# Kernel tuning notes

Hardware: AMD Instinct MI355X
Metric: run time of the kernel (lower is better)

Reference implementation:

```python
import jax, jax.numpy as jnp
import numpy as np

# Block structure (mirrors init_kwargs)
K = 8            # number of blocks
BLK = 1024       # per-block in/out width
TOTAL = K * BLK  # total_dim = 8192
INPUT_IDX = [(i * BLK, (i + 1) * BLK) for i in range(K)]
OUTPUT_IDX = [(((i + 1) % K) * BLK, ((i + 1) % K + 1) * BLK) for i in range(K)]
BATCH = 4096


def setup_inputs() -> dict:
    key = jax.random.key(0)
    k1, k2, k3, k4 = jax.random.split(key, 4)
    x = jax.random.normal(k1, (BATCH, TOTAL), dtype=jnp.float32)
    v = jax.random.normal(k2, (BATCH, TOTAL), dtype=jnp.float32)
    # Per-block Linear params; nn.Linear default init ~ U(-1/sqrt(in), 1/sqrt(in))
    bound = 1.0 / np.sqrt(BLK)
    W = jax.random.uniform(k3, (K, BLK, BLK), dtype=jnp.float32, minval=-bound, maxval=bound)  # [K, out, in]
    b = jax.random.uniform(k4, (K, BLK), dtype=jnp.float32, minval=-bound, maxval=bound)
    return {"x": x, "v": v, "W": W, "b": b}


def reference(x, v, W, b):
    # hidden = act(v)
    hidden = jnp.tanh(v)
    # All input blocks are a uniform partition -> batch the K small GEMMs as one grouped contraction.
    h = hidden.reshape(BATCH, K, BLK)                      # [B, K, in]
    y = jnp.einsum("bki,koi->bko", h, W) + b               # [B, K, out]
    # Scatter-accumulate each block output into its padded position, plus residual x.
    result = x
    for i, (o0, o1) in enumerate(OUTPUT_IDX):
        result = result.at[:, o0:o1].add(y[:, i])
    return result
```

## Files before the change

kernel.cpp:

```cpp
#include <hip/hip_runtime.h>
#include <hip/hip_bf16.h>
#include <stdint.h>

#define BATCH 4096
#define KGRP  8
#define BLK   1024
#define TOTAL 8192

typedef __attribute__((ext_vector_type(8))) short short8;
typedef __attribute__((ext_vector_type(4))) float f32x4;

#define AS1 __attribute__((address_space(1)))
#define AS3 __attribute__((address_space(3)))


__device__ __forceinline__ unsigned short f2bf(float f) {
    union { float f; uint32_t u; } c; c.f = f;
    uint32_t u = c.u;
    u += 0x7fffu + ((u >> 16) & 1u);
    return (unsigned short)(u >> 16);
}

__device__ __forceinline__ float fast_tanh(float x) {
    float e = __expf(2.0f * x);
    return 1.0f - 2.0f / (e + 1.0f);
}


__global__ void k_prep(const float4* __restrict__ v, ushort4* __restrict__ H,
                       const float4* __restrict__ W, ushort4* __restrict__ Wb) {
    const int b = blockIdx.x;
    if (b < 2048) {
        const int n4 = BATCH * TOTAL / 4;
        for (int i = b * 256 + threadIdx.x; i < n4; i += 2048 * 256) {
            float4 f = v[i];
            ushort4 o;
            o.x = f2bf(fast_tanh(f.x)); o.y = f2bf(fast_tanh(f.y));
            o.z = f2bf(fast_tanh(f.z)); o.w = f2bf(fast_tanh(f.w));
            H[i] = o;
        }
    } else {
        const int n4 = KGRP * BLK * BLK / 4;
        for (int i = (b - 2048) * 256 + threadIdx.x; i < n4; i += 512 * 256) {
            float4 f = W[i];
            ushort4 o;
            o.x = f2bf(f.x); o.y = f2bf(f.y); o.z = f2bf(f.z); o.w = f2bf(f.w);
            Wb[i] = o;
        }
    }
}


__device__ __forceinline__ void gload16(const unsigned short* src, char* dst) {
    __builtin_amdgcn_global_load_lds((const AS1 uint32_t*)src, (AS3 uint32_t*)dst, 16, 0, 0);
}

template<int N> __device__ __forceinline__ void waitvm() {
    if constexpr (N == 0)      asm volatile("s_waitcnt vmcnt(0)" ::: "memory");
    else if constexpr (N == 2) asm volatile("s_waitcnt vmcnt(2)" ::: "memory");
    else if constexpr (N == 3) asm volatile("s_waitcnt vmcnt(3)" ::: "memory");
}

template<bool SA, bool SB, int W>
__device__ __forceinline__ void tile_body(int kt, char* ldsp,
                                          uint32_t aRowB, uint32_t bRowB, uint32_t kc,
                                          f32x4 (*acc)[4],
                                          const unsigned short* Asrc, const unsigned short* Bsrc,
                                          uint32_t sdst) {
    const uint32_t bufb = (uint32_t)(kt & 1) * 24576u;
    const uint32_t nbuf = bufb ^ 24576u;
    const char* Lb = ldsp + bufb;

    short8 bfr[4], am[2];

#pragma unroll
    for (int n = 0; n < 4; ++n)
        bfr[n] = *(const short8*)(Lb + bRowB + n * 1024 + kc);
#pragma unroll
    for (int i = 0; i < 2; ++i)
        am[i] = *(const short8*)(Lb + aRowB + i * 1024 + kc);
    if constexpr (SA) gload16(Asrc + (kt + 1) * 32, ldsp + nbuf + sdst);
#pragma unroll
    for (int i = 0; i < 2; ++i)
#pragma unroll
        for (int n = 0; n < 4; ++n)
            acc[i][n] = __builtin_amdgcn_mfma_f32_16x16x32_bf16(am[i], bfr[n], acc[i][n], 0, 0, 0);
    __builtin_amdgcn_s_barrier();
    __builtin_amdgcn_sched_barrier(0);

#pragma unroll
    for (int i = 0; i < 2; ++i)
        am[i] = *(const short8*)(Lb + aRowB + (2 + i) * 1024 + kc);
    if constexpr (SB) {
        gload16(Bsrc + (kt + 2) * 32, ldsp + bufb + 8192u + sdst);
        gload16(Bsrc + (size_t)128 * BLK + (kt + 2) * 32, ldsp + bufb + 16384u + sdst);
    }
#pragma unroll
    for (int i = 0; i < 2; ++i)
#pragma unroll
        for (int n = 0; n < 4; ++n)
            acc[2 + i][n] = __builtin_amdgcn_mfma_f32_16x16x32_bf16(am[i], bfr[n], acc[2 + i][n], 0, 0, 0);
    if constexpr (W >= 0) {
        waitvm<W>();
        __builtin_amdgcn_s_barrier();
        __builtin_amdgcn_sched_barrier(0);
    }
}

__global__ __launch_bounds__(512, 4)
void k_gemm(const unsigned short* __restrict__ H, const unsigned short* __restrict__ Wb,
            const float* __restrict__ x, const float* __restrict__ bias,
            float* __restrict__ out) {
    __shared__ __attribute__((aligned(1024))) char lds[49152];
    char* ldsp = lds;

    const int bid   = blockIdx.x;
    const int g     = bid & 7;
    const int slot  = bid >> 3;
    const int mtile = slot >> 2;
    const int ntile = slot & 3;

    const int tid  = threadIdx.x;
    const int lane = tid & 63;
    const int w    = tid >> 6;
    const int wr   = w >> 2;
    const int wc   = w & 3;

    const uint32_t kc    = ((uint32_t)((lane >> 4) ^ ((lane >> 1) & 3))) << 4;
    const uint32_t aRowB = (uint32_t)(wr * 64 + (lane & 15)) * 64u;
    const uint32_t bRowB = 8192u + (uint32_t)(wc * 64 + (lane & 15)) * 64u;

    const int sCol = ((lane & 3) ^ ((lane >> 3) & 3)) << 3;
    const unsigned short* Asrc = H + (size_t)(mtile * 128 + w * 16 + (lane >> 2)) * TOTAL
                                   + (size_t)g * BLK + sCol;
    const unsigned short* Bsrc = Wb + (size_t)g * BLK * BLK
                                    + (size_t)(ntile * 256 + w * 16 + (lane >> 2)) * BLK + sCol;
    const uint32_t sdst = (uint32_t)(w << 10);

    f32x4 acc[4][4];
#pragma unroll
    for (int m = 0; m < 4; ++m)
#pragma unroll
        for (int n = 0; n < 4; ++n) acc[m][n] = (f32x4){0.f, 0.f, 0.f, 0.f};

    gload16(Asrc + 0 * 32, ldsp + 0u + sdst);
    gload16(Bsrc + 0 * 32, ldsp + 8192u + sdst);
    gload16(Bsrc + (size_t)128 * BLK + 0 * 32, ldsp + 16384u + sdst);
    gload16(Asrc + 1 * 32, ldsp + 24576u + sdst);
    gload16(Bsrc + 1 * 32, ldsp + 24576u + 8192u + sdst);
    gload16(Bsrc + (size_t)128 * BLK + 1 * 32, ldsp + 24576u + 16384u + sdst);
    waitvm<3>();
    __builtin_amdgcn_s_barrier();
    __builtin_amdgcn_sched_barrier(0);

    tile_body<false, true, 2>(0, ldsp, aRowB, bRowB, kc, acc, Asrc, Bsrc, sdst);
#pragma unroll 1
    for (int kt = 1; kt < 30; ++kt)
        tile_body<true, true, 2>(kt, ldsp, aRowB, bRowB, kc, acc, Asrc, Bsrc, sdst);
    tile_body<true, false, 0>(30, ldsp, aRowB, bRowB, kc, acc, Asrc, Bsrc, sdst);
    tile_body<false, false, -1>(31, ldsp, aRowB, bRowB, kc, acc, Asrc, Bsrc, sdst);

    __builtin_amdgcn_s_barrier();

    const int gout = (g + 1) & 7;
    const int q    = lane >> 4;
    const int cl   = lane & 15;
    const int row0 = mtile * 128 + wr * 64;
    const int col0 = ntile * 256 + wc * 64;
    char* eb = ldsp + (uint32_t)w * 4352u;
    const float4 bias4 = *(const float4*)&bias[g * BLK + col0 + cl * 4];

#pragma unroll
    for (int m = 0; m < 4; ++m) {
#pragma unroll
        for (int n = 0; n < 4; ++n)
#pragma unroll
            for (int j = 0; j < 4; ++j)
                *(float*)(eb + (q * 4 + j) * 272 + (n * 16 + cl) * 4) = acc[m][n][j];
        asm volatile("s_waitcnt lgkmcnt(0)" ::: "memory");
        __builtin_amdgcn_sched_barrier(0);
#pragma unroll
        for (int i = 0; i < 4; ++i) {
            f32x4 vv = *(const f32x4*)(eb + (q + 4 * i) * 272 + cl * 16);
            const int r = row0 + m * 16 + q + 4 * i;
            const size_t idx = (size_t)r * TOTAL + (size_t)gout * BLK + col0 + cl * 4;
            const float4 xv = *(const float4*)&x[idx];
            float4 o;
            o.x = xv.x + bias4.x + vv[0];
            o.y = xv.y + bias4.y + vv[1];
            o.z = xv.z + bias4.z + vv[2];
            o.w = xv.w + bias4.w + vv[3];
            *(float4*)&out[idx] = o;
        }
        asm volatile("s_waitcnt lgkmcnt(0)" ::: "memory");
        __builtin_amdgcn_sched_barrier(0);
    }
}


__global__ void k_naive(const float* __restrict__ x, const float* __restrict__ v,
                        const float* __restrict__ W, const float* __restrict__ b,
                        float* __restrict__ out) {
    __shared__ float hv[BLK];
    const int bid = blockIdx.x;
    const int quarter = bid & 3;
    const int g = (bid >> 2) & 7;
    const int row = bid >> 5;
    for (int i = threadIdx.x; i < BLK; i += 256)
        hv[i] = tanhf(v[(size_t)row * TOTAL + g * BLK + i]);
    __syncthreads();
    const int o = quarter * 256 + threadIdx.x;
    const float* wrow = W + ((size_t)g * BLK + o) * BLK;
    float s = 0.f;
    for (int i = 0; i < BLK; ++i) s += hv[i] * wrow[i];
    const size_t oi = (size_t)row * TOTAL + (size_t)((g + 1) & 7) * BLK + o;
    out[oi] = x[oi] + b[g * BLK + o] + s;
}


extern "C" void kernel_launch(void* const* d_in, const int* in_sizes, int n_in,
                              void* d_out, int out_size, void* d_ws, size_t ws_size,
                              hipStream_t stream) {
    const float* x = (const float*)d_in[0];
    const float* v = (const float*)d_in[1];
    const float* W = (const float*)d_in[2];
    const float* b = (const float*)d_in[3];
    float* out = (float*)d_out;

    const size_t needH = (size_t)BATCH * TOTAL * sizeof(unsigned short);
    const size_t needW = (size_t)KGRP * BLK * BLK * sizeof(unsigned short);

    if (ws_size >= needH + needW) {
        unsigned short* H  = (unsigned short*)d_ws;
        unsigned short* Wb = (unsigned short*)((char*)d_ws + needH);
        k_prep<<<2560, 256, 0, stream>>>((const float4*)v, (ushort4*)H,
                                         (const float4*)W, (ushort4*)Wb);
        k_gemm<<<1024, 512, 0, stream>>>(H, Wb, x, b, out);
    } else {
        k_naive<<<BATCH * KGRP * 4, 256, 0, stream>>>(x, v, W, b, out);
    }
}
```

Baseline: 163.7 us.

## Switch GEMM main loop to triple-buffered LDS with one barrier per tile

Replaces the double-buffered K loop, which had two barriers per tile and split A/B staging, with a three-stage LDS ring. Each tile issues all loads for tile kt+2 up front, reads all fragments, then runs the 16 MFMAs under raised wave priority (s_setprio). The loop is unrolled by three with compile-time buffer offsets, and the swizzle offset is folded into the row base addresses. LDS use rises from 48KB to 72KB per block, which may reduce how many blocks fit on a CU relative to the launch bound of 4.

```diff
diff --git a/kernel.cpp b/kernel.cpp
--- a/kernel.cpp
+++ b/kernel.cpp
@@ -57,49 +57,49 @@
 
 template<int N> __device__ __forceinline__ void waitvm() {
     if constexpr (N == 0)      asm volatile("s_waitcnt vmcnt(0)" ::: "memory");
-    else if constexpr (N == 2) asm volatile("s_waitcnt vmcnt(2)" ::: "memory");
     else if constexpr (N == 3) asm volatile("s_waitcnt vmcnt(3)" ::: "memory");
 }
 
-template<bool SA, bool SB, int W>
-__device__ __forceinline__ void tile_body(int kt, char* ldsp,
-                                          uint32_t aRowB, uint32_t bRowB, uint32_t kc,
-                                          f32x4 (*acc)[4],
-                                          const unsigned short* Asrc, const unsigned short* Bsrc,
-                                          uint32_t sdst) {
-    const uint32_t bufb = (uint32_t)(kt & 1) * 24576u;
-    const uint32_t nbuf = bufb ^ 24576u;
+template<bool ST, int W, int CUR>
+__device__ __forceinline__ void tile3(int kt, char* ldsp,
+                                      uint32_t aRowB, uint32_t bRowB,
+                                      f32x4 (*acc)[4],
+                                      const unsigned short* Asrc, const unsigned short* Bsrc,
+                                      uint32_t sdst) {
+    constexpr uint32_t bufb = (uint32_t)(CUR * 24576);
+    constexpr uint32_t stgb = (uint32_t)(((CUR + 2) % 3) * 24576);
     const char* Lb = ldsp + bufb;
 
-    short8 bfr[4], am[2];
-
+    if constexpr (ST) {
+        gload16(Asrc + (size_t)(kt + 2) * 32, ldsp + stgb + sdst);
+        gload16(Bsrc + (size_t)(kt + 2) * 32, ldsp + stgb + 8192u + sdst);
+        gload16(Bsrc + (size_t)128 * BLK + (size_t)(kt + 2) * 32, ldsp + stgb + 16384u + sdst);
+    }
+
+    short8 bfr[4], am0[2], am1[2];
 #pragma unroll
     for (int n = 0; n < 4; ++n)
-        bfr[n] = *(const short8*)(Lb + bRowB + n * 1024 + kc);
-#pragma unroll
-    for (int i = 0; i < 2; ++i)
-        am[i] = *(const short8*)(Lb + aRowB + i * 1024 + kc);
-    if constexpr (SA) gload16(Asrc + (kt + 1) * 32, ldsp + nbuf + sdst);
+        bfr[n] = *(const short8*)(Lb + bRowB + n * 1024);
+#pragma unroll
+    for (int i = 0; i < 2; ++i)
+        am0[i] = *(const short8*)(Lb + aRowB + i * 1024);
+#pragma unroll
+    for (int i = 0; i < 2; ++i)
+        am1[i] = *(const short8*)(Lb + aRowB + (2 + i) * 1024);
+
+    __builtin_amdgcn_s_setprio(1);
 #pragma unroll
     for (int i = 0; i < 2; ++i)
 #pragma unroll
         for (int n = 0; n < 4; ++n)
-            acc[i][n] = __builtin_amdgcn_mfma_f32_16x16x32_bf16(am[i], bfr[n], acc[i][n], 0, 0, 0);
-    __builtin_amdgcn_s_barrier();
-    __builtin_amdgcn_sched_barrier(0);
-
-#pragma unroll
-    for (int i = 0; i < 2; ++i)
-        am[i] = *(const short8*)(Lb + aRowB + (2 + i) * 1024 + kc);
-    if constexpr (SB) {
-        gload16(Bsrc + (kt + 2) * 32, ldsp + bufb + 8192u + sdst);
-        gload16(Bsrc + (size_t)128 * BLK + (kt + 2) * 32, ldsp + bufb + 16384u + sdst);
-    }
+            acc[i][n] = __builtin_amdgcn_mfma_f32_16x16x32_bf16(am0[i], bfr[n], acc[i][n], 0, 0, 0);
 #pragma unroll
     for (int i = 0; i < 2; ++i)
 #pragma unroll
         for (int n = 0; n < 4; ++n)
-            acc[2 + i][n] = __builtin_amdgcn_mfma_f32_16x16x32_bf16(am[i], bfr[n], acc[2 + i][n], 0, 0, 0);
+            acc[2 + i][n] = __builtin_amdgcn_mfma_f32_16x16x32_bf16(am1[i], bfr[n], acc[2 + i][n], 0, 0, 0);
+    __builtin_amdgcn_s_setprio(0);
+
     if constexpr (W >= 0) {
         waitvm<W>();
         __builtin_amdgcn_s_barrier();
@@ -111,7 +111,7 @@
 void k_gemm(const unsigned short* __restrict__ H, const unsigned short* __restrict__ Wb,
             const float* __restrict__ x, const float* __restrict__ bias,
             float* __restrict__ out) {
-    __shared__ __attribute__((aligned(1024))) char lds[49152];
+    __shared__ __attribute__((aligned(1024))) char lds[73728];
     char* ldsp = lds;
 
     const int bid   = blockIdx.x;
@@ -127,8 +127,8 @@
     const int wc   = w & 3;
 
     const uint32_t kc    = ((uint32_t)((lane >> 4) ^ ((lane >> 1) & 3))) << 4;
-    const uint32_t aRowB = (uint32_t)(wr * 64 + (lane & 15)) * 64u;
-    const uint32_t bRowB = 8192u + (uint32_t)(wc * 64 + (lane & 15)) * 64u;
+    const uint32_t aRowB = (uint32_t)(wr * 64 + (lane & 15)) * 64u + kc;
+    const uint32_t bRowB = 8192u + (uint32_t)(wc * 64 + (lane & 15)) * 64u + kc;
 
     const int sCol = ((lane & 3) ^ ((lane >> 3) & 3)) << 3;
     const unsigned short* Asrc = H + (size_t)(mtile * 128 + w * 16 + (lane >> 2)) * TOTAL
@@ -143,22 +143,24 @@
 #pragma unroll
         for (int n = 0; n < 4; ++n) acc[m][n] = (f32x4){0.f, 0.f, 0.f, 0.f};
 
-    gload16(Asrc + 0 * 32, ldsp + 0u + sdst);
-    gload16(Bsrc + 0 * 32, ldsp + 8192u + sdst);
-    gload16(Bsrc + (size_t)128 * BLK + 0 * 32, ldsp + 16384u + sdst);
-    gload16(Asrc + 1 * 32, ldsp + 24576u + sdst);
-    gload16(Bsrc + 1 * 32, ldsp + 24576u + 8192u + sdst);
-    gload16(Bsrc + (size_t)128 * BLK + 1 * 32, ldsp + 24576u + 16384u + sdst);
+    gload16(Asrc + 0, ldsp + 0u + sdst);
+    gload16(Bsrc + 0, ldsp + 8192u + sdst);
+    gload16(Bsrc + (size_t)128 * BLK, ldsp + 16384u + sdst);
+    gload16(Asrc + 32, ldsp + 24576u + sdst);
+    gload16(Bsrc + 32, ldsp + 24576u + 8192u + sdst);
+    gload16(Bsrc + (size_t)128 * BLK + 32, ldsp + 24576u + 16384u + sdst);
     waitvm<3>();
     __builtin_amdgcn_s_barrier();
     __builtin_amdgcn_sched_barrier(0);
 
-    tile_body<false, true, 2>(0, ldsp, aRowB, bRowB, kc, acc, Asrc, Bsrc, sdst);
 #pragma unroll 1
-    for (int kt = 1; kt < 30; ++kt)
-        tile_body<true, true, 2>(kt, ldsp, aRowB, bRowB, kc, acc, Asrc, Bsrc, sdst);
-    tile_body<true, false, 0>(30, ldsp, aRowB, bRowB, kc, acc, Asrc, Bsrc, sdst);
-    tile_body<false, false, -1>(31, ldsp, aRowB, bRowB, kc, acc, Asrc, Bsrc, sdst);
+    for (int kt = 0; kt < 30; kt += 3) {
+        tile3<true, 3, 0>(kt,     ldsp, aRowB, bRowB, acc, Asrc, Bsrc, sdst);
+        tile3<true, 3, 1>(kt + 1, ldsp, aRowB, bRowB, acc, Asrc, Bsrc, sdst);
+        tile3<true, 3, 2>(kt + 2, ldsp, aRowB, bRowB, acc, Asrc, Bsrc, sdst);
+    }
+    tile3<false, 0, 0>(30, ldsp, aRowB, bRowB, acc, Asrc, Bsrc, sdst);
+    tile3<false, -1, 1>(31, ldsp, aRowB, bRowB, acc, Asrc, Bsrc, sdst);
 
     __builtin_amdgcn_s_barrier();
 
```

Result: faster. 157.7 us (-3.7%).

## Fuse tanh and bf16 cast of v into GEMM A-tile loading

Applied to the files above, without the earlier changes.

Removes the separate prep pass that wrote a bf16 tanh(v) buffer to memory. The GEMM now loads fp32 v directly into registers three tiles ahead, applies tanh and bf16 conversion, and writes the A tile into LDS itself, while weights are still cast by a small separate kernel. This drops a full write and re-read of the activation intermediate. In exchange A loads double in bytes and go through registers instead of direct-to-LDS. Each ntile re-reads v, so tanh is recomputed 4x, and s_setprio hints are added around MFMA blocks.

```diff
diff --git a/kernel.cpp b/kernel.cpp
--- a/kernel.cpp
+++ b/kernel.cpp
@@ -26,31 +26,6 @@
     return 1.0f - 2.0f / (e + 1.0f);
 }
 
-
-__global__ void k_prep(const float4* __restrict__ v, ushort4* __restrict__ H,
-                       const float4* __restrict__ W, ushort4* __restrict__ Wb) {
-    const int b = blockIdx.x;
-    if (b < 2048) {
-        const int n4 = BATCH * TOTAL / 4;
-        for (int i = b * 256 + threadIdx.x; i < n4; i += 2048 * 256) {
-            float4 f = v[i];
-            ushort4 o;
-            o.x = f2bf(fast_tanh(f.x)); o.y = f2bf(fast_tanh(f.y));
-            o.z = f2bf(fast_tanh(f.z)); o.w = f2bf(fast_tanh(f.w));
-            H[i] = o;
-        }
-    } else {
-        const int n4 = KGRP * BLK * BLK / 4;
-        for (int i = (b - 2048) * 256 + threadIdx.x; i < n4; i += 512 * 256) {
-            float4 f = W[i];
-            ushort4 o;
-            o.x = f2bf(f.x); o.y = f2bf(f.y); o.z = f2bf(f.z); o.w = f2bf(f.w);
-            Wb[i] = o;
-        }
-    }
-}
-
-
 __device__ __forceinline__ void gload16(const unsigned short* src, char* dst) {
     __builtin_amdgcn_global_load_lds((const AS1 uint32_t*)src, (AS3 uint32_t*)dst, 16, 0, 0);
 }
@@ -58,49 +33,79 @@
 template<int N> __device__ __forceinline__ void waitvm() {
     if constexpr (N == 0)      asm volatile("s_waitcnt vmcnt(0)" ::: "memory");
     else if constexpr (N == 2) asm volatile("s_waitcnt vmcnt(2)" ::: "memory");
-    else if constexpr (N == 3) asm volatile("s_waitcnt vmcnt(3)" ::: "memory");
-}
-
-template<bool SA, bool SB, int W>
-__device__ __forceinline__ void tile_body(int kt, char* ldsp,
-                                          uint32_t aRowB, uint32_t bRowB, uint32_t kc,
-                                          f32x4 (*acc)[4],
-                                          const unsigned short* Asrc, const unsigned short* Bsrc,
-                                          uint32_t sdst) {
-    const uint32_t bufb = (uint32_t)(kt & 1) * 24576u;
-    const uint32_t nbuf = bufb ^ 24576u;
-    const char* Lb = ldsp + bufb;
+    else if constexpr (N == 4) asm volatile("s_waitcnt vmcnt(4)" ::: "memory");
+    else if constexpr (N == 6) asm volatile("s_waitcnt vmcnt(6)" ::: "memory");
+}
+
+
+__global__ void k_wcast(const float4* __restrict__ W, ushort4* __restrict__ Wb) {
+    const int n4 = KGRP * BLK * BLK / 4;
+    for (int i = blockIdx.x * 256 + threadIdx.x; i < n4; i += 1024 * 256) {
+        float4 f = W[i];
+        ushort4 o;
+        o.x = f2bf(f.x); o.y = f2bf(f.y); o.z = f2bf(f.z); o.w = f2bf(f.w);
+        Wb[i] = o;
+    }
+}
+
+
+template<bool WRA, bool ISSV, bool ISSB, int W>
+__device__ __forceinline__ void tile_f(int kt, char* ldsp,
+                                       uint32_t aRd, uint32_t bRd, uint32_t aWr,
+                                       const float* vsrc, const unsigned short* BsrcT,
+                                       uint32_t sdstB,
+                                       float4& vc0, float4& vc1,
+                                       f32x4 (*acc)[4]) {
+    const uint32_t cur = (uint32_t)(kt & 1) * 24576u;
+    const uint32_t oth = cur ^ 24576u;
+    const char* Lb = ldsp + cur;
 
     short8 bfr[4], am[2];
 
 #pragma unroll
     for (int n = 0; n < 4; ++n)
-        bfr[n] = *(const short8*)(Lb + bRowB + n * 1024 + kc);
-#pragma unroll
-    for (int i = 0; i < 2; ++i)
-        am[i] = *(const short8*)(Lb + aRowB + i * 1024 + kc);
-    if constexpr (SA) gload16(Asrc + (kt + 1) * 32, ldsp + nbuf + sdst);
+        bfr[n] = *(const short8*)(Lb + bRd + n * 1024);
+#pragma unroll
+    for (int i = 0; i < 2; ++i)
+        am[i] = *(const short8*)(Lb + aRd + i * 1024);
+    if constexpr (WRA) {
+        short8 p;
+        p[0] = (short)f2bf(fast_tanh(vc0.x)); p[1] = (short)f2bf(fast_tanh(vc0.y));
+        p[2] = (short)f2bf(fast_tanh(vc0.z)); p[3] = (short)f2bf(fast_tanh(vc0.w));
+        p[4] = (short)f2bf(fast_tanh(vc1.x)); p[5] = (short)f2bf(fast_tanh(vc1.y));
+        p[6] = (short)f2bf(fast_tanh(vc1.z)); p[7] = (short)f2bf(fast_tanh(vc1.w));
+        *(short8*)(ldsp + oth + aWr) = p;
+    }
+    if constexpr (ISSV) {
+        vc0 = *(const float4*)(vsrc + (kt + 3) * 32);
+        vc1 = *(const float4*)(vsrc + (kt + 3) * 32 + 4);
+    }
+    __builtin_amdgcn_s_setprio(1);
 #pragma unroll
     for (int i = 0; i < 2; ++i)
 #pragma unroll
         for (int n = 0; n < 4; ++n)
             acc[i][n] = __builtin_amdgcn_mfma_f32_16x16x32_bf16(am[i], bfr[n], acc[i][n], 0, 0, 0);
+    __builtin_amdgcn_s_setprio(0);
     __builtin_amdgcn_s_barrier();
     __builtin_amdgcn_sched_barrier(0);
 
 #pragma unroll
     for (int i = 0; i < 2; ++i)
-        am[i] = *(const short8*)(Lb + aRowB + (2 + i) * 1024 + kc);
-    if constexpr (SB) {
-        gload16(Bsrc + (kt + 2) * 32, ldsp + bufb + 8192u + sdst);
-        gload16(Bsrc + (size_t)128 * BLK + (kt + 2) * 32, ldsp + bufb + 16384u + sdst);
-    }
+        am[i] = *(const short8*)(Lb + aRd + (2 + i) * 1024);
+    if constexpr (ISSB) {
+        gload16(BsrcT + (size_t)(kt + 2) * 32, ldsp + cur + 8192u + sdstB);
+        gload16(BsrcT + (size_t)128 * BLK + (size_t)(kt + 2) * 32, ldsp + cur + 16384u + sdstB);
+    }
+    __builtin_amdgcn_s_setprio(1);
 #pragma unroll
     for (int i = 0; i < 2; ++i)
 #pragma unroll
         for (int n = 0; n < 4; ++n)
             acc[2 + i][n] = __builtin_amdgcn_mfma_f32_16x16x32_bf16(am[i], bfr[n], acc[2 + i][n], 0, 0, 0);
+    __builtin_amdgcn_s_setprio(0);
     if constexpr (W >= 0) {
+        asm volatile("s_waitcnt lgkmcnt(0)" ::: "memory");
         waitvm<W>();
         __builtin_amdgcn_s_barrier();
         __builtin_amdgcn_sched_barrier(0);
@@ -108,7 +113,7 @@
 }
 
 __global__ __launch_bounds__(512, 4)
-void k_gemm(const unsigned short* __restrict__ H, const unsigned short* __restrict__ Wb,
+void k_main(const float* __restrict__ v, const unsigned short* __restrict__ Wb,
             const float* __restrict__ x, const float* __restrict__ bias,
             float* __restrict__ out) {
     __shared__ __attribute__((aligned(1024))) char lds[49152];
@@ -119,6 +124,7 @@
     const int slot  = bid >> 3;
     const int mtile = slot >> 2;
     const int ntile = slot & 3;
+    const int gout  = (g + 1) & 7;
 
     const int tid  = threadIdx.x;
     const int lane = tid & 63;
@@ -126,16 +132,19 @@
     const int wr   = w >> 2;
     const int wc   = w & 3;
 
-    const uint32_t kc    = ((uint32_t)((lane >> 4) ^ ((lane >> 1) & 3))) << 4;
-    const uint32_t aRowB = (uint32_t)(wr * 64 + (lane & 15)) * 64u;
-    const uint32_t bRowB = 8192u + (uint32_t)(wc * 64 + (lane & 15)) * 64u;
-
-    const int sCol = ((lane & 3) ^ ((lane >> 3) & 3)) << 3;
-    const unsigned short* Asrc = H + (size_t)(mtile * 128 + w * 16 + (lane >> 2)) * TOTAL
-                                   + (size_t)g * BLK + sCol;
-    const unsigned short* Bsrc = Wb + (size_t)g * BLK * BLK
-                                    + (size_t)(ntile * 256 + w * 16 + (lane >> 2)) * BLK + sCol;
-    const uint32_t sdst = (uint32_t)(w << 10);
+    const uint32_t kc  = ((uint32_t)((lane >> 4) ^ ((lane >> 1) & 3))) << 4;
+    const uint32_t aRd = (uint32_t)(wr * 64 + (lane & 15)) * 64u + kc;
+    const uint32_t bRd = 8192u + (uint32_t)(wc * 64 + (lane & 15)) * 64u + kc;
+
+    const uint32_t aWr = (uint32_t)(tid >> 2) * 64u +
+                         (((uint32_t)((tid & 3) ^ ((tid >> 3) & 3))) << 4);
+    const float* vsrc = v + (size_t)(mtile * 128 + (tid >> 2)) * TOTAL
+                          + (size_t)g * BLK + (tid & 3) * 8;
+
+    const int sColB = ((lane & 3) ^ ((lane >> 3) & 3)) << 3;
+    const unsigned short* BsrcT = Wb + (size_t)g * BLK * BLK
+                                     + (size_t)(ntile * 256 + w * 16 + (lane >> 2)) * BLK + sColB;
+    const uint32_t sdstB = (uint32_t)(w << 10);
 
     f32x4 acc[4][4];
 #pragma unroll
@@ -143,28 +152,41 @@
 #pragma unroll
         for (int n = 0; n < 4; ++n) acc[m][n] = (f32x4){0.f, 0.f, 0.f, 0.f};
 
-    gload16(Asrc + 0 * 32, ldsp + 0u + sdst);
-    gload16(Bsrc + 0 * 32, ldsp + 8192u + sdst);
-    gload16(Bsrc + (size_t)128 * BLK + 0 * 32, ldsp + 16384u + sdst);
-    gload16(Asrc + 1 * 32, ldsp + 24576u + sdst);
-    gload16(Bsrc + 1 * 32, ldsp + 24576u + 8192u + sdst);
-    gload16(Bsrc + (size_t)128 * BLK + 1 * 32, ldsp + 24576u + 16384u + sdst);
-    waitvm<3>();
+    gload16(BsrcT, ldsp + 8192u + sdstB);
+    gload16(BsrcT + (size_t)128 * BLK, ldsp + 16384u + sdstB);
+    gload16(BsrcT + 32, ldsp + 24576u + 8192u + sdstB);
+    gload16(BsrcT + (size_t)128 * BLK + 32, ldsp + 24576u + 16384u + sdstB);
+    float4 t0a = *(const float4*)(vsrc);
+    float4 t0b = *(const float4*)(vsrc + 4);
+    float4 vA0 = *(const float4*)(vsrc + 32), vA1 = *(const float4*)(vsrc + 36);
+    float4 vB0 = *(const float4*)(vsrc + 64), vB1 = *(const float4*)(vsrc + 68);
+    {
+        short8 p;
+        p[0] = (short)f2bf(fast_tanh(t0a.x)); p[1] = (short)f2bf(fast_tanh(t0a.y));
+        p[2] = (short)f2bf(fast_tanh(t0a.z)); p[3] = (short)f2bf(fast_tanh(t0a.w));
+        p[4] = (short)f2bf(fast_tanh(t0b.x)); p[5] = (short)f2bf(fast_tanh(t0b.y));
+        p[6] = (short)f2bf(fast_tanh(t0b.z)); p[7] = (short)f2bf(fast_tanh(t0b.w));
+        *(short8*)(ldsp + aWr) = p;
+    }
+    asm volatile("s_waitcnt lgkmcnt(0)" ::: "memory");
+    waitvm<6>();
     __builtin_amdgcn_s_barrier();
     __builtin_amdgcn_sched_barrier(0);
 
-    tile_body<false, true, 2>(0, ldsp, aRowB, bRowB, kc, acc, Asrc, Bsrc, sdst);
 #pragma unroll 1
-    for (int kt = 1; kt < 30; ++kt)
-        tile_body<true, true, 2>(kt, ldsp, aRowB, bRowB, kc, acc, Asrc, Bsrc, sdst);
-    tile_body<true, false, 0>(30, ldsp, aRowB, bRowB, kc, acc, Asrc, Bsrc, sdst);
-    tile_body<false, false, -1>(31, ldsp, aRowB, bRowB, kc, acc, Asrc, Bsrc, sdst);
+    for (int k2 = 0; k2 < 14; ++k2) {
+        tile_f<true, true, true, 4>(2 * k2,     ldsp, aRd, bRd, aWr, vsrc, BsrcT, sdstB, vA0, vA1, acc);
+        tile_f<true, true, true, 4>(2 * k2 + 1, ldsp, aRd, bRd, aWr, vsrc, BsrcT, sdstB, vB0, vB1, acc);
+    }
+    tile_f<true, true,  true,  4>(28, ldsp, aRd, bRd, aWr, vsrc, BsrcT, sdstB, vA0, vA1, acc);
+    tile_f<true, false, true,  2>(29, ldsp, aRd, bRd, aWr, vsrc, BsrcT, sdstB, vB0, vB1, acc);
+    tile_f<true, false, false, 0>(30, ldsp, aRd, bRd, aWr, vsrc, BsrcT, sdstB, vA0, vA1, acc);
+    tile_f<false, false, false, -1>(31, ldsp, aRd, bRd, aWr, vsrc, BsrcT, sdstB, vB0, vB1, acc);
 
     __builtin_amdgcn_s_barrier();
 
-    const int gout = (g + 1) & 7;
-    const int q    = lane >> 4;
-    const int cl   = lane & 15;
+    const int q  = lane >> 4;
+    const int cl = lane & 15;
     const int row0 = mtile * 128 + wr * 64;
     const int col0 = ntile * 256 + wc * 64;
     char* eb = ldsp + (uint32_t)w * 4352u;
@@ -227,15 +249,12 @@
     const float* b = (const float*)d_in[3];
     float* out = (float*)d_out;
 
-    const size_t needH = (size_t)BATCH * TOTAL * sizeof(unsigned short);
     const size_t needW = (size_t)KGRP * BLK * BLK * sizeof(unsigned short);
 
-    if (ws_size >= needH + needW) {
-        unsigned short* H  = (unsigned short*)d_ws;
-        unsigned short* Wb = (unsigned short*)((char*)d_ws + needH);
-        k_prep<<<2560, 256, 0, stream>>>((const float4*)v, (ushort4*)H,
-                                         (const float4*)W, (ushort4*)Wb);
-        k_gemm<<<1024, 512, 0, stream>>>(H, Wb, x, b, out);
+    if (ws_size >= needW) {
+        unsigned short* Wb = (unsigned short*)d_ws;
+        k_wcast<<<1024, 256, 0, stream>>>((const float4*)W, (ushort4*)Wb);
+        k_main<<<1024, 512, 0, stream>>>(v, Wb, x, b, out);
     } else {
         k_naive<<<BATCH * KGRP * 4, 256, 0, stream>>>(x, v, W, b, out);
     }
```

Measured after the change: 174.5 us. 1.07x slower.
